# Kernel tuning notes

Measured on AMD Instinct MI355X. Metric: run time of the kernel, lower is better.

Reference implementation:

```python
import jax, jax.numpy as jnp
import numpy as np

B, T, C = 128, 512, 1024  # batch, time (fixed by `line` buffer), channels


def fft_convolve(a, b):
    """Linear convolution via zero-padded FFT, sliced to a's length.
    a: (1, C, T) kernel, b: (B, C, T) signal. Returns (B, C, T)."""
    n = a.shape[-1]
    a_pad = jnp.pad(a, ((0, 0), (0, 0), (0, n)))
    b_pad = jnp.pad(b, ((0, 0), (0, 0), (0, n)))
    spec = jnp.fft.rfft(a_pad, axis=-1) * jnp.fft.rfft(b_pad, axis=-1)
    return jnp.fft.irfft(spec, n=2 * n, axis=-1)[..., :n]


def setup_inputs() -> dict:
    key = jax.random.key(0)
    k1, k2, k3, k4, k5 = jax.random.split(key, 5)
    bound = 1.0 / np.sqrt(C)  # nn.Linear default init range
    x = jax.random.normal(k1, (B, T, C), dtype=jnp.float32)
    W_proj = jax.random.uniform(k2, (C, C), jnp.float32, -bound, bound)
    W_values = jax.random.uniform(k3, (C, C), jnp.float32, -bound, bound)
    gain = jax.random.uniform(k4, (1, 1, C), jnp.float32, 0.01, 1.0)
    pow_ = jax.random.uniform(k5, (1, C, 1), jnp.float32, -6.0, 6.0)
    line = jnp.linspace(1.0, 0.0, T, dtype=jnp.float32)[None, None, :]  # (1,1,T)
    return {"x": x, "W_proj": W_proj, "W_values": W_values,
            "gain": gain, "pow_": pow_, "line": line}


def reference(x, W_proj, W_values, gain, pow_, line):
    # proj and values (bias-free Linears)
    h = jnp.einsum('btc,dc->btd', x, W_proj)          # (B,T,C)
    v = jnp.einsum('btc,dc->btd', h, W_values)        # (B,T,C)
    # learned power-law kernel, one decay per channel: (1,C,T)
    z = line ** (2.0 + jax.nn.sigmoid(pow_) * 100.0)
    # FFT long convolution along time
    y = fft_convolve(z, jnp.transpose(v, (0, 2, 1)))  # (B,C,T)
    y = jnp.transpose(y, (0, 2, 1))                    # (B,T,C)
    return jax.nn.relu(y * gain)
```

## Files before the change

### kernel.cpp

```cpp
#include <hip/hip_runtime.h>
#include <hip/hip_bf16.h>

#define B_ 128
#define T_ 512
#define C_ 1024

typedef __attribute__((ext_vector_type(8))) short short8;
typedef __attribute__((ext_vector_type(4))) float f32x4;

__device__ __forceinline__ unsigned short f2bf(float f){
  unsigned u; __builtin_memcpy(&u, &f, 4);
  u += 0x7FFFu + ((u >> 16) & 1u);
  return (unsigned short)(u >> 16);
}

typedef __attribute__((address_space(3))) unsigned lds_u32_t;
typedef __attribute__((address_space(1))) unsigned glb_u32_t;
typedef __attribute__((address_space(3))) char lds_char;
__device__ __forceinline__ void gload16(const void* g, void* l){
  __builtin_amdgcn_global_load_lds((const glb_u32_t*)g, (lds_u32_t*)l, 16, 0, 0);
}

__global__ void cast_f32_bf16(const float* __restrict__ in, unsigned short* __restrict__ out, long n){
  long i = (long)blockIdx.x * blockDim.x + threadIdx.x;
  long stride = (long)gridDim.x * blockDim.x;
  for (long j = i * 4; j < n; j += stride * 4){
    float4 v = *(const float4*)(in + j);
    ushort4 o; o.x = f2bf(v.x); o.y = f2bf(v.y); o.z = f2bf(v.z); o.w = f2bf(v.w);
    *(ushort4*)(out + j) = o;
  }
}

__global__ void transpose_cast(const float* __restrict__ in, unsigned short* __restrict__ out){
  __shared__ float tile[32][33];
  int c0 = blockIdx.x * 32, e0 = blockIdx.y * 32;
  int tx = threadIdx.x, ty = threadIdx.y;
  for (int r = 0; r < 32; r += 8)
    tile[ty + r][tx] = in[(size_t)(e0 + ty + r) * C_ + c0 + tx];
  __syncthreads();
  for (int r = 0; r < 32; r += 8)
    out[(size_t)(c0 + ty + r) * C_ + e0 + tx] = f2bf(tile[tx][ty + r]);
}

__global__ __launch_bounds__(256) void gemm_bt_bf16(
    const unsigned short* __restrict__ A,
    const unsigned short* __restrict__ Bt,
    unsigned short* __restrict__ Cc,
    int M, int N, int K)
{
  __shared__ short As[128 * 32];
  __shared__ short Bs[128 * 32];
  const int tid  = threadIdx.x;
  const int lane = tid & 63;
  const int wave = tid >> 6;
  const int wr = wave >> 1, wc = wave & 1;
  const int lr = lane & 15, kg = lane >> 4;
  const int m0 = blockIdx.x * 128;
  const int n0 = blockIdx.y * 128;

  f32x4 acc[4][4];
  #pragma unroll
  for (int mi = 0; mi < 4; mi++)
    #pragma unroll
    for (int ni = 0; ni < 4; ni++)
      acc[mi][ni] = (f32x4){0.f, 0.f, 0.f, 0.f};

  const int r1 = tid >> 2, ch1 = tid & 3;
  char* abase = (char*)As + (tid & ~63) * 16;
  char* bbase = (char*)Bs + (tid & ~63) * 16;

  for (int k0 = 0; k0 < K; k0 += 32){
    __syncthreads();
    gload16(A  + (size_t)(m0 + r1)      * K + k0 + ch1 * 8, abase);
    gload16(A  + (size_t)(m0 + 64 + r1) * K + k0 + ch1 * 8, abase + 4096);
    gload16(Bt + (size_t)(n0 + r1)      * K + k0 + ch1 * 8, bbase);
    gload16(Bt + (size_t)(n0 + 64 + r1) * K + k0 + ch1 * 8, bbase + 4096);
    __syncthreads();

    short8 af[4], bfr[4];
    #pragma unroll
    for (int mi = 0; mi < 4; mi++)
      af[mi] = *(const short8*)&As[(wr * 64 + mi * 16 + lr) * 32 + kg * 8];
    #pragma unroll
    for (int ni = 0; ni < 4; ni++)
      bfr[ni] = *(const short8*)&Bs[(wc * 64 + ni * 16 + lr) * 32 + kg * 8];
    #pragma unroll
    for (int mi = 0; mi < 4; mi++)
      #pragma unroll
      for (int ni = 0; ni < 4; ni++)
        acc[mi][ni] = __builtin_amdgcn_mfma_f32_16x16x32_bf16(af[mi], bfr[ni], acc[mi][ni], 0, 0, 0);
  }

  #pragma unroll
  for (int mi = 0; mi < 4; mi++)
    #pragma unroll
    for (int ni = 0; ni < 4; ni++){
      int n = n0 + wc * 64 + ni * 16 + lr;
      int mb = m0 + wr * 64 + mi * 16 + kg * 4;
      #pragma unroll
      for (int j = 0; j < 4; j++)
        Cc[(size_t)(mb + j) * N + n] = f2bf(acc[mi][ni][j]);
    }
}

#define SWZ(x) ((x) ^ ((((x) >> 7) & 3) << 4))

#define STAGE_B(kt, kh) { \
  int d_ = wv * 1024 + ln * 16; int o_ = SWZ(d_); \
  gload16(Bg + (size_t)(n0 + (o_ >> 6)) * 1024 + (kt) * 64 + (kh) * 32 + ((o_ >> 4) & 3) * 8, \
          ldsc + 65536 + ((kt) & 1) * 32768 + (kh) * 16384 + wv * 1024); \
  d_ += 8192; o_ = SWZ(d_); \
  gload16(Bg + (size_t)(n0 + (o_ >> 6)) * 1024 + (kt) * 64 + (kh) * 32 + ((o_ >> 4) & 3) * 8, \
          ldsc + 65536 + ((kt) & 1) * 32768 + (kh) * 16384 + 8192 + wv * 1024); }

#define LOADA(kt) { \
  _Pragma("unroll") for (int kh = 0; kh < 2; kh++) \
    _Pragma("unroll") for (int hf = 0; hf < 2; hf++){ \
      const float* p_ = Ag32 + (size_t)(m0 + rowA + hf * 128) * 1024 + (kt) * 64 + kh * 32 + c8 * 8; \
      areg[kh][hf][0] = *(const float4*)p_; \
      areg[kh][hf][1] = *(const float4*)(p_ + 4); } }

#define CVTWRITE(slot) { \
  _Pragma("unroll") for (int kh = 0; kh < 2; kh++) \
    _Pragma("unroll") for (int hf = 0; hf < 2; hf++){ \
      short8 w_; \
      _Pragma("unroll") for (int q = 0; q < 4; q++){ \
        w_[q]     = (short)f2bf(areg[kh][hf][0][q]); \
        w_[q + 4] = (short)f2bf(areg[kh][hf][1][q]); } \
      int d_ = wv * 1024 + ln * 16 + hf * 8192; \
      unsigned ad_ = (unsigned)(size_t)(lds3 + (slot) * 32768 + kh * 16384 + SWZ(d_)); \
      asm volatile("ds_write_b128 %0, %1" :: "v"(ad_), "v"(w_)); } }

__global__ __launch_bounds__(512, 2) void gemm256_fused(
    const float* __restrict__ Ag32,
    const unsigned short* __restrict__ Bg,
    unsigned short* __restrict__ vt)
{
  extern __shared__ char ldsc[];
  lds_char* lds3 = (lds_char*)ldsc;
  const int tid = threadIdx.x;
  const int ln  = tid & 63;
  const int wv  = tid >> 6;
  const int wr  = wv >> 2;
  const int wc  = wv & 3;
  const int lr  = ln & 15, kg = ln >> 4;
  const int rowA = wv * 16 + (ln >> 2);
  const int c8   = ln & 3;
  const int id  = blockIdx.x;
  const int jj  = (id & 7) * 128 + (id >> 3);
  const int n0  = (jj & 3) * 256;
  const int m0  = (jj >> 2) * 256;

  f32x4 acc[8][4];
  #pragma unroll
  for (int mi = 0; mi < 8; mi++)
    #pragma unroll
    for (int ni = 0; ni < 4; ni++)
      acc[mi][ni] = (f32x4){0.f, 0.f, 0.f, 0.f};

  float4 areg[2][2][2];

  LOADA(0);
  asm volatile("s_waitcnt vmcnt(0)");
  __builtin_amdgcn_sched_barrier(0);
  CVTWRITE(0);
  __builtin_amdgcn_sched_barrier(0);
  STAGE_B(0, 0); STAGE_B(0, 1);
  __builtin_amdgcn_sched_barrier(0);
  asm volatile("s_waitcnt lgkmcnt(0)");
  __builtin_amdgcn_sched_barrier(0);
  asm volatile("s_waitcnt vmcnt(0)");
  __builtin_amdgcn_sched_barrier(0);
  __builtin_amdgcn_s_barrier();

  short8 af[8], bfr[4];

  #pragma unroll 1
  for (int t = 0; t < 16; ++t){
    const int S = t & 1;

    if (t < 15){
      LOADA(t + 1);
      __builtin_amdgcn_sched_barrier(0);
      STAGE_B(t + 1, 0); STAGE_B(t + 1, 1);
      __builtin_amdgcn_sched_barrier(0);
    }

    #pragma unroll
    for (int mi = 0; mi < 8; mi++){
      int off = S * 32768 + (wr * 128 + mi * 16 + lr) * 64 + kg * 16;
      unsigned a_ = (unsigned)(size_t)(lds3 + SWZ(off));
      asm volatile("ds_read_b128 %0, %1" : "=v"(af[mi]) : "v"(a_));
    }
    #pragma unroll
    for (int ni = 0; ni < 4; ni++){
      int off = 65536 + S * 32768 + (wc * 64 + ni * 16 + lr) * 64 + kg * 16;
      unsigned a_ = (unsigned)(size_t)(lds3 + SWZ(off));
      asm volatile("ds_read_b128 %0, %1" : "=v"(bfr[ni]) : "v"(a_));
    }
    asm volatile("s_waitcnt lgkmcnt(0)");
    __builtin_amdgcn_sched_barrier(0);
    __builtin_amdgcn_s_setprio(1);
    #pragma unroll
    for (int mi = 0; mi < 8; mi++)
      #pragma unroll
      for (int ni = 0; ni < 4; ni++)
        acc[mi][ni] = __builtin_amdgcn_mfma_f32_16x16x32_bf16(af[mi], bfr[ni], acc[mi][ni], 0, 0, 0);
    __builtin_amdgcn_s_setprio(0);
    __builtin_amdgcn_sched_barrier(0);

    #pragma unroll
    for (int mi = 0; mi < 8; mi++){
      int off = S * 32768 + 16384 + (wr * 128 + mi * 16 + lr) * 64 + kg * 16;
      unsigned a_ = (unsigned)(size_t)(lds3 + SWZ(off));
      asm volatile("ds_read_b128 %0, %1" : "=v"(af[mi]) : "v"(a_));
    }
    #pragma unroll
    for (int ni = 0; ni < 4; ni++){
      int off = 65536 + S * 32768 + 16384 + (wc * 64 + ni * 16 + lr) * 64 + kg * 16;
      unsigned a_ = (unsigned)(size_t)(lds3 + SWZ(off));
      asm volatile("ds_read_b128 %0, %1" : "=v"(bfr[ni]) : "v"(a_));
    }
    asm volatile("s_waitcnt lgkmcnt(0)");
    __builtin_amdgcn_sched_barrier(0);
    __builtin_amdgcn_s_setprio(1);
    #pragma unroll
    for (int mi = 0; mi < 8; mi++)
      #pragma unroll
      for (int ni = 0; ni < 4; ni++)
        acc[mi][ni] = __builtin_amdgcn_mfma_f32_16x16x32_bf16(af[mi], bfr[ni], acc[mi][ni], 0, 0, 0);
    __builtin_amdgcn_s_setprio(0);
    __builtin_amdgcn_sched_barrier(0);

    if (t < 15){
      asm volatile("s_waitcnt vmcnt(0)");
      __builtin_amdgcn_sched_barrier(0);
      CVTWRITE(S ^ 1);
      __builtin_amdgcn_sched_barrier(0);
      asm volatile("s_waitcnt lgkmcnt(0)");
      __builtin_amdgcn_sched_barrier(0);
    }
    __builtin_amdgcn_s_barrier();
  }

  #pragma unroll
  for (int mi = 0; mi < 8; mi++)
    #pragma unroll
    for (int ni = 0; ni < 4; ni++){
      int n  = n0 + wc * 64 + ni * 16 + lr;
      int mb = m0 + wr * 128 + mi * 16 + kg * 4;
      int bb = mb >> 9, t = mb & 511;
      ushort4 o;
      o.x = f2bf(acc[mi][ni][0]); o.y = f2bf(acc[mi][ni][1]);
      o.z = f2bf(acc[mi][ni][2]); o.w = f2bf(acc[mi][ni][3]);
      *(ushort4*)&vt[((size_t)n * B_ + bb) * T_ + t] = o;
    }
}

__global__ __launch_bounds__(256) void conv_mfma(
    const unsigned short* __restrict__ vt,
    const float* __restrict__ pw,
    const float* __restrict__ line,
    const float* __restrict__ gain,
    unsigned short* __restrict__ Ybf)
{
  __shared__ short Bs[128 * 32];
  __shared__ short Ab[16 * 1280];
  __shared__ unsigned short zbuf[512];
  const int id  = blockIdx.x;
  const int xcd = id & 7;
  const int jj  = id >> 3;
  const int c   = xcd + ((jj >> 2) << 3);
  const int t0  = (jj & 3) << 7;
  const int tid = threadIdx.x, lane = tid & 63, wave = tid >> 6;
  const int wr = wave >> 1, wc = wave & 1, lr = lane & 15, kg = lane >> 4;
  const int K  = t0 + 128;
  const int nb = (t0 >> 5) + 4;

  {
    float p = pw[c];
    float e = 2.0f + 100.0f / (1.0f + expf(-p));
    for (int k = tid; k < K; k += 256){
      float lv = line[k];
      float z = (lv > 0.f) ? expf(e * logf(lv)) : 0.f;
      zbuf[k] = f2bf(z);
    }
  }
  __syncthreads();
  for (int idx = tid; idx < nb * 1280; idx += 256){
    int i = idx / 40, j = idx - i * 40;
    int d32 = i >> 5, ii = i & 31;
    int k = d32 * 32 + ii - j;
    unsigned short v = 0;
    if (j < 32 && k >= 0) v = zbuf[k];
    Ab[idx] = v;
  }

  f32x4 acc[4][4];
  #pragma unroll
  for (int mi = 0; mi < 4; mi++)
    #pragma unroll
    for (int ni = 0; ni < 4; ni++)
      acc[mi][ni] = (f32x4){0.f, 0.f, 0.f, 0.f};

  const int r1 = tid >> 2, ch1 = tid & 3;
  char* bbase = (char*)Bs + (tid & ~63) * 16;
  const size_t vbase = (size_t)c * B_ * T_;

  for (int k0 = 0; k0 < K; k0 += 32){
    __syncthreads();
    gload16(vt + vbase + (size_t)r1 * T_        + k0 + ch1 * 8, bbase);
    gload16(vt + vbase + (size_t)(64 + r1) * T_ + k0 + ch1 * 8, bbase + 4096);
    __syncthreads();

    short8 bfr[4];
    #pragma unroll
    for (int ni = 0; ni < 4; ni++)
      bfr[ni] = *(const short8*)&Bs[(wc * 64 + ni * 16 + lr) * 32 + kg * 8];

    const int dbase = ((t0 - k0) >> 5) + wr * 2;
    #pragma unroll
    for (int mi = 0; mi < 4; mi++){
      const int d32 = dbase + (mi >> 1);
      if (d32 >= 0){
        const int i = ((mi & 1) << 4) + lr;
        short8 af = *(const short8*)&Ab[d32 * 1280 + i * 40 + kg * 8];
        #pragma unroll
        for (int ni = 0; ni < 4; ni++)
          acc[mi][ni] = __builtin_amdgcn_mfma_f32_16x16x32_bf16(af, bfr[ni], acc[mi][ni], 0, 0, 0);
      }
    }
  }

  const float g = gain[c];
  #pragma unroll
  for (int mi = 0; mi < 4; mi++)
    #pragma unroll
    for (int ni = 0; ni < 4; ni++){
      int t = t0 + wr * 64 + mi * 16 + kg * 4;
      int b = wc * 64 + ni * 16 + lr;
      ushort4 o;
      o.x = f2bf(fmaxf(acc[mi][ni][0] * g, 0.f));
      o.y = f2bf(fmaxf(acc[mi][ni][1] * g, 0.f));
      o.z = f2bf(fmaxf(acc[mi][ni][2] * g, 0.f));
      o.w = f2bf(fmaxf(acc[mi][ni][3] * g, 0.f));
      *(ushort4*)&Ybf[((size_t)c * B_ + b) * T_ + t] = o;
    }
}

__global__ __launch_bounds__(256) void final_out(const unsigned short* __restrict__ Ybf,
                                                 float* __restrict__ out){
  __shared__ unsigned short tile[64][72];
  const int c0 = blockIdx.x * 64;
  const int t0 = blockIdx.y * 64;
  const int b  = blockIdx.z;
  const int tid = threadIdx.x;
  const int cr = tid >> 4;
  const int t4 = (tid & 15) * 4;
  for (int q = 0; q < 64; q += 16){
    ushort4 u = *(const ushort4*)&Ybf[((size_t)(c0 + cr + q) * B_ + b) * T_ + t0 + t4];
    *(ushort4*)&tile[cr + q][t4] = u;
  }
  __syncthreads();
  const int tr = tid >> 4;
  const int c4 = (tid & 15) * 4;
  for (int q = 0; q < 64; q += 16){
    int t = tr + q;
    float4 o;
    o.x = __uint_as_float((unsigned)tile[c4 + 0][t] << 16);
    o.y = __uint_as_float((unsigned)tile[c4 + 1][t] << 16);
    o.z = __uint_as_float((unsigned)tile[c4 + 2][t] << 16);
    o.w = __uint_as_float((unsigned)tile[c4 + 3][t] << 16);
    *(float4*)&out[((size_t)b * T_ + t0 + t) * C_ + c0 + c4] = o;
  }
}

extern "C" void kernel_launch(void* const* d_in, const int* in_sizes, int n_in,
                              void* d_out, int out_size, void* d_ws, size_t ws_size,
                              hipStream_t stream)
{
  (void)in_sizes; (void)n_in; (void)out_size; (void)ws_size;
  const float* x    = (const float*)d_in[0];
  const float* Wp   = (const float*)d_in[1];
  const float* Wv   = (const float*)d_in[2];
  const float* gain = (const float*)d_in[3];
  const float* pw   = (const float*)d_in[4];
  const float* line = (const float*)d_in[5];
  float* out = (float*)d_out;

  char* ws = (char*)d_ws;
  unsigned short* Ybf   = (unsigned short*)ws;
  unsigned short* WpT   = (unsigned short*)(ws + 134217728);
  unsigned short* Wv_bf = (unsigned short*)(ws + 134217728 + 2097152);
  unsigned short* W_f   = (unsigned short*)(ws + 134217728 + 2 * 2097152);
  unsigned short* vt    = (unsigned short*)d_out + 67108864;

  cast_f32_bf16<<<256, 256, 0, stream>>>(Wv, Wv_bf, (long)C_ * C_);
  transpose_cast<<<dim3(32, 32), dim3(32, 8), 0, stream>>>(Wp, WpT);
  gemm_bt_bf16<<<dim3(8, 8), 256, 0, stream>>>(Wv_bf, WpT, W_f, C_, C_, C_);
  gemm256_fused<<<1024, 512, 131072, stream>>>(x, W_f, vt);
  conv_mfma<<<4096, 256, 0, stream>>>(vt, pw, line, gain, Ybf);
  final_out<<<dim3(16, 8, 128), 256, 0, stream>>>(Ybf, out);
}
```

Baseline: 447.1 us.

## Pair conv time tiles per block and interleave LDS reads with MFMAs

The causal-convolution kernel now has each block compute two 128-step output tiles, pairing tiles 0 with 2 and 1 with 3. The shared input stream is loaded once and feeds both accumulator sets, which halves the grid, cuts redundant vt loads and Toeplitz setup, and evens out the triangular work per block. The price is double the accumulator registers, which may lower occupancy. In the main GEMM, each half-K step now issues its B then A LDS reads and begins MFMAs per A fragment using staged lgkmcnt waits, so LDS latency overlaps with compute.

Measured after the change: 508.8 us. +13.8%, slower.

```diff
diff --git a/kernel.cpp b/kernel.cpp
--- a/kernel.cpp
+++ b/kernel.cpp
@@ -130,6 +130,32 @@
       int d_ = wv * 1024 + ln * 16 + hf * 8192; \
       unsigned ad_ = (unsigned)(size_t)(lds3 + (slot) * 32768 + kh * 16384 + SWZ(d_)); \
       asm volatile("ds_write_b128 %0, %1" :: "v"(ad_), "v"(w_)); } }
+
+#define MFMA4(MI) { \
+  acc[MI][0] = __builtin_amdgcn_mfma_f32_16x16x32_bf16(af[MI], bfr[0], acc[MI][0], 0, 0, 0); \
+  acc[MI][1] = __builtin_amdgcn_mfma_f32_16x16x32_bf16(af[MI], bfr[1], acc[MI][1], 0, 0, 0); \
+  acc[MI][2] = __builtin_amdgcn_mfma_f32_16x16x32_bf16(af[MI], bfr[2], acc[MI][2], 0, 0, 0); \
+  acc[MI][3] = __builtin_amdgcn_mfma_f32_16x16x32_bf16(af[MI], bfr[3], acc[MI][3], 0, 0, 0); }
+
+#define LSTEP(N, MI) { \
+  asm volatile("s_waitcnt lgkmcnt(" #N ")"); \
+  __builtin_amdgcn_sched_barrier(0); \
+  MFMA4(MI); }
+
+#define KHALF(S, KHOFF) { \
+  _Pragma("unroll") for (int ni = 0; ni < 4; ni++){ \
+    int off = 65536 + (S) * 32768 + (KHOFF) + (wc * 64 + ni * 16 + lr) * 64 + kg * 16; \
+    unsigned a_ = (unsigned)(size_t)(lds3 + SWZ(off)); \
+    asm volatile("ds_read_b128 %0, %1" : "=v"(bfr[ni]) : "v"(a_)); } \
+  _Pragma("unroll") for (int mi = 0; mi < 8; mi++){ \
+    int off = (S) * 32768 + (KHOFF) + (wr * 128 + mi * 16 + lr) * 64 + kg * 16; \
+    unsigned a_ = (unsigned)(size_t)(lds3 + SWZ(off)); \
+    asm volatile("ds_read_b128 %0, %1" : "=v"(af[mi]) : "v"(a_)); } \
+  __builtin_amdgcn_s_setprio(1); \
+  LSTEP(7, 0) LSTEP(6, 1) LSTEP(5, 2) LSTEP(4, 3) \
+  LSTEP(3, 4) LSTEP(2, 5) LSTEP(1, 6) LSTEP(0, 7) \
+  __builtin_amdgcn_s_setprio(0); \
+  __builtin_amdgcn_sched_barrier(0); }
 
 __global__ __launch_bounds__(512, 2) void gemm256_fused(
     const float* __restrict__ Ag32,
@@ -186,51 +212,8 @@
       __builtin_amdgcn_sched_barrier(0);
     }
 
-    #pragma unroll
-    for (int mi = 0; mi < 8; mi++){
-      int off = S * 32768 + (wr * 128 + mi * 16 + lr) * 64 + kg * 16;
-      unsigned a_ = (unsigned)(size_t)(lds3 + SWZ(off));
-      asm volatile("ds_read_b128 %0, %1" : "=v"(af[mi]) : "v"(a_));
-    }
-    #pragma unroll
-    for (int ni = 0; ni < 4; ni++){
-      int off = 65536 + S * 32768 + (wc * 64 + ni * 16 + lr) * 64 + kg * 16;
-      unsigned a_ = (unsigned)(size_t)(lds3 + SWZ(off));
-      asm volatile("ds_read_b128 %0, %1" : "=v"(bfr[ni]) : "v"(a_));
-    }
-    asm volatile("s_waitcnt lgkmcnt(0)");
-    __builtin_amdgcn_sched_barrier(0);
-    __builtin_amdgcn_s_setprio(1);
-    #pragma unroll
-    for (int mi = 0; mi < 8; mi++)
-      #pragma unroll
-      for (int ni = 0; ni < 4; ni++)
-        acc[mi][ni] = __builtin_amdgcn_mfma_f32_16x16x32_bf16(af[mi], bfr[ni], acc[mi][ni], 0, 0, 0);
-    __builtin_amdgcn_s_setprio(0);
-    __builtin_amdgcn_sched_barrier(0);
-
-    #pragma unroll
-    for (int mi = 0; mi < 8; mi++){
-      int off = S * 32768 + 16384 + (wr * 128 + mi * 16 + lr) * 64 + kg * 16;
-      unsigned a_ = (unsigned)(size_t)(lds3 + SWZ(off));
-      asm volatile("ds_read_b128 %0, %1" : "=v"(af[mi]) : "v"(a_));
-    }
-    #pragma unroll
-    for (int ni = 0; ni < 4; ni++){
-      int off = 65536 + S * 32768 + 16384 + (wc * 64 + ni * 16 + lr) * 64 + kg * 16;
-      unsigned a_ = (unsigned)(size_t)(lds3 + SWZ(off));
-      asm volatile("ds_read_b128 %0, %1" : "=v"(bfr[ni]) : "v"(a_));
-    }
-    asm volatile("s_waitcnt lgkmcnt(0)");
-    __builtin_amdgcn_sched_barrier(0);
-    __builtin_amdgcn_s_setprio(1);
-    #pragma unroll
-    for (int mi = 0; mi < 8; mi++)
-      #pragma unroll
-      for (int ni = 0; ni < 4; ni++)
-        acc[mi][ni] = __builtin_amdgcn_mfma_f32_16x16x32_bf16(af[mi], bfr[ni], acc[mi][ni], 0, 0, 0);
-    __builtin_amdgcn_s_setprio(0);
-    __builtin_amdgcn_sched_barrier(0);
+    KHALF(S, 0)
+    KHALF(S, 16384)
 
     if (t < 15){
       asm volatile("s_waitcnt vmcnt(0)");
@@ -257,7 +240,7 @@
     }
 }
 
-__global__ __launch_bounds__(256) void conv_mfma(
+__global__ __launch_bounds__(256) void conv_mfma2(
     const unsigned short* __restrict__ vt,
     const float* __restrict__ pw,
     const float* __restrict__ line,
@@ -270,17 +253,19 @@
   const int id  = blockIdx.x;
   const int xcd = id & 7;
   const int jj  = id >> 3;
-  const int c   = xcd + ((jj >> 2) << 3);
-  const int t0  = (jj & 3) << 7;
+  const int c   = xcd + ((jj >> 1) << 3);
+  const int pr  = jj & 1;
+  const int t0b = pr ? 384 : 128;
+  const int t0a = t0b - 128;
+  const int Kp  = t0b + 128;
   const int tid = threadIdx.x, lane = tid & 63, wave = tid >> 6;
   const int wr = wave >> 1, wc = wave & 1, lr = lane & 15, kg = lane >> 4;
-  const int K  = t0 + 128;
-  const int nb = (t0 >> 5) + 4;
+  const int nb = (t0b >> 5) + 4;
 
   {
     float p = pw[c];
     float e = 2.0f + 100.0f / (1.0f + expf(-p));
-    for (int k = tid; k < K; k += 256){
+    for (int k = tid; k < Kp; k += 256){
       float lv = line[k];
       float z = (lv > 0.f) ? expf(e * logf(lv)) : 0.f;
       zbuf[k] = f2bf(z);
@@ -296,18 +281,20 @@
     Ab[idx] = v;
   }
 
-  f32x4 acc[4][4];
+  f32x4 acca[4][4], accb[4][4];
   #pragma unroll
   for (int mi = 0; mi < 4; mi++)
     #pragma unroll
-    for (int ni = 0; ni < 4; ni++)
-      acc[mi][ni] = (f32x4){0.f, 0.f, 0.f, 0.f};
+    for (int ni = 0; ni < 4; ni++){
+      acca[mi][ni] = (f32x4){0.f, 0.f, 0.f, 0.f};
+      accb[mi][ni] = (f32x4){0.f, 0.f, 0.f, 0.f};
+    }
 
   const int r1 = tid >> 2, ch1 = tid & 3;
   char* bbase = (char*)Bs + (tid & ~63) * 16;
   const size_t vbase = (size_t)c * B_ * T_;
 
-  for (int k0 = 0; k0 < K; k0 += 32){
+  for (int k0 = 0; k0 < Kp; k0 += 32){
     __syncthreads();
     gload16(vt + vbase + (size_t)r1 * T_        + k0 + ch1 * 8, bbase);
     gload16(vt + vbase + (size_t)(64 + r1) * T_ + k0 + ch1 * 8, bbase + 4096);
@@ -318,18 +305,34 @@
     for (int ni = 0; ni < 4; ni++)
       bfr[ni] = *(const short8*)&Bs[(wc * 64 + ni * 16 + lr) * 32 + kg * 8];
 
-    const int dbase = ((t0 - k0) >> 5) + wr * 2;
-    #pragma unroll
-    for (int mi = 0; mi < 4; mi++){
-      const int d32 = dbase + (mi >> 1);
-      if (d32 >= 0){
-        const int i = ((mi & 1) << 4) + lr;
-        short8 af = *(const short8*)&Ab[d32 * 1280 + i * 40 + kg * 8];
-        #pragma unroll
-        for (int ni = 0; ni < 4; ni++)
-          acc[mi][ni] = __builtin_amdgcn_mfma_f32_16x16x32_bf16(af, bfr[ni], acc[mi][ni], 0, 0, 0);
+    {
+      const int dbase = ((t0b - k0) >> 5) + wr * 2;
+      #pragma unroll
+      for (int mi = 0; mi < 4; mi++){
+        const int d32 = dbase + (mi >> 1);
+        if (d32 >= 0){
+          const int i = ((mi & 1) << 4) + lr;
+          short8 afv = *(const short8*)&Ab[d32 * 1280 + i * 40 + kg * 8];
+          #pragma unroll
+          for (int ni = 0; ni < 4; ni++)
+            accb[mi][ni] = __builtin_amdgcn_mfma_f32_16x16x32_bf16(afv, bfr[ni], accb[mi][ni], 0, 0, 0);
+        }
       }
     }
+    if (k0 < t0b){
+      const int dbase = ((t0a - k0) >> 5) + wr * 2;
+      #pragma unroll
+      for (int mi = 0; mi < 4; mi++){
+        const int d32 = dbase + (mi >> 1);
+        if (d32 >= 0){
+          const int i = ((mi & 1) << 4) + lr;
+          short8 afv = *(const short8*)&Ab[d32 * 1280 + i * 40 + kg * 8];
+          #pragma unroll
+          for (int ni = 0; ni < 4; ni++)
+            acca[mi][ni] = __builtin_amdgcn_mfma_f32_16x16x32_bf16(afv, bfr[ni], acca[mi][ni], 0, 0, 0);
+        }
+      }
+    }
   }
 
   const float g = gain[c];
@@ -337,14 +340,20 @@
   for (int mi = 0; mi < 4; mi++)
     #pragma unroll
     for (int ni = 0; ni < 4; ni++){
-      int t = t0 + wr * 64 + mi * 16 + kg * 4;
       int b = wc * 64 + ni * 16 + lr;
-      ushort4 o;
-      o.x = f2bf(fmaxf(acc[mi][ni][0] * g, 0.f));
-      o.y = f2bf(fmaxf(acc[mi][ni][1] * g, 0.f));
-      o.z = f2bf(fmaxf(acc[mi][ni][2] * g, 0.f));
-      o.w = f2bf(fmaxf(acc[mi][ni][3] * g, 0.f));
-      *(ushort4*)&Ybf[((size_t)c * B_ + b) * T_ + t] = o;
+      int ta = t0a + wr * 64 + mi * 16 + kg * 4;
+      int tb = t0b + wr * 64 + mi * 16 + kg * 4;
+      ushort4 oa, ob;
+      oa.x = f2bf(fmaxf(acca[mi][ni][0] * g, 0.f));
+      oa.y = f2bf(fmaxf(acca[mi][ni][1] * g, 0.f));
+      oa.z = f2bf(fmaxf(acca[mi][ni][2] * g, 0.f));
+      oa.w = f2bf(fmaxf(acca[mi][ni][3] * g, 0.f));
+      ob.x = f2bf(fmaxf(accb[mi][ni][0] * g, 0.f));
+      ob.y = f2bf(fmaxf(accb[mi][ni][1] * g, 0.f));
+      ob.z = f2bf(fmaxf(accb[mi][ni][2] * g, 0.f));
+      ob.w = f2bf(fmaxf(accb[mi][ni][3] * g, 0.f));
+      *(ushort4*)&Ybf[((size_t)c * B_ + b) * T_ + ta] = oa;
+      *(ushort4*)&Ybf[((size_t)c * B_ + b) * T_ + tb] = ob;
     }
 }
 
@@ -399,6 +408,6 @@
   transpose_cast<<<dim3(32, 32), dim3(32, 8), 0, stream>>>(Wp, WpT);
   gemm_bt_bf16<<<dim3(8, 8), 256, 0, stream>>>(Wv_bf, WpT, W_f, C_, C_, C_);
   gemm256_fused<<<1024, 512, 131072, stream>>>(x, W_f, vt);
-  conv_mfma<<<4096, 256, 0, stream>>>(vt, pw, line, gain, Ybf);
+  conv_mfma2<<<2048, 256, 0, stream>>>(vt, pw, line, gain, Ybf);
   final_out<<<dim3(16, 8, 128), 256, 0, stream>>>(Ybf, out);
 }
```

## Interleave LDS reads with MFMAs in GEMM and register-prefetch conv tiles

Applied to the files above, without the earlier changes.

In the main GEMM, each K-half now issues its B-fragment reads and then its A-fragment reads, and the MFMA rows start under progressively shrinking lgkmcnt waits, so matrix math begins before every LDS read has landed. The convolution kernel stops using direct global-to-LDS loads with two block barriers per step. It now prefetches the next vt tile into registers during the current step's compute and writes it to LDS at the start of the next step. It also hoists the Toeplitz A-fragment reads ahead of the MFMAs, clamping negative diagonal indices so the reads need no branch. The aim is to hide LDS and global latency behind MFMA work, at the cost of more registers and the added inline-asm ordering constraints.

New measurement: 437.9 us. 1.02x faster.

```diff
diff --git a/kernel.cpp b/kernel.cpp
--- a/kernel.cpp
+++ b/kernel.cpp
@@ -130,6 +130,32 @@
       int d_ = wv * 1024 + ln * 16 + hf * 8192; \
       unsigned ad_ = (unsigned)(size_t)(lds3 + (slot) * 32768 + kh * 16384 + SWZ(d_)); \
       asm volatile("ds_write_b128 %0, %1" :: "v"(ad_), "v"(w_)); } }
+
+#define MFMA4(MI) { \
+  acc[MI][0] = __builtin_amdgcn_mfma_f32_16x16x32_bf16(af[MI], bfr[0], acc[MI][0], 0, 0, 0); \
+  acc[MI][1] = __builtin_amdgcn_mfma_f32_16x16x32_bf16(af[MI], bfr[1], acc[MI][1], 0, 0, 0); \
+  acc[MI][2] = __builtin_amdgcn_mfma_f32_16x16x32_bf16(af[MI], bfr[2], acc[MI][2], 0, 0, 0); \
+  acc[MI][3] = __builtin_amdgcn_mfma_f32_16x16x32_bf16(af[MI], bfr[3], acc[MI][3], 0, 0, 0); }
+
+#define LSTEP(N, MI) { \
+  asm volatile("s_waitcnt lgkmcnt(" #N ")"); \
+  __builtin_amdgcn_sched_barrier(0); \
+  MFMA4(MI); }
+
+#define KHALF(S, KHOFF) { \
+  _Pragma("unroll") for (int ni = 0; ni < 4; ni++){ \
+    int off = 65536 + (S) * 32768 + (KHOFF) + (wc * 64 + ni * 16 + lr) * 64 + kg * 16; \
+    unsigned a_ = (unsigned)(size_t)(lds3 + SWZ(off)); \
+    asm volatile("ds_read_b128 %0, %1" : "=v"(bfr[ni]) : "v"(a_)); } \
+  _Pragma("unroll") for (int mi = 0; mi < 8; mi++){ \
+    int off = (S) * 32768 + (KHOFF) + (wr * 128 + mi * 16 + lr) * 64 + kg * 16; \
+    unsigned a_ = (unsigned)(size_t)(lds3 + SWZ(off)); \
+    asm volatile("ds_read_b128 %0, %1" : "=v"(af[mi]) : "v"(a_)); } \
+  __builtin_amdgcn_s_setprio(1); \
+  LSTEP(7, 0) LSTEP(6, 1) LSTEP(5, 2) LSTEP(4, 3) \
+  LSTEP(3, 4) LSTEP(2, 5) LSTEP(1, 6) LSTEP(0, 7) \
+  __builtin_amdgcn_s_setprio(0); \
+  __builtin_amdgcn_sched_barrier(0); }
 
 __global__ __launch_bounds__(512, 2) void gemm256_fused(
     const float* __restrict__ Ag32,
@@ -186,51 +212,8 @@
       __builtin_amdgcn_sched_barrier(0);
     }
 
-    #pragma unroll
-    for (int mi = 0; mi < 8; mi++){
-      int off = S * 32768 + (wr * 128 + mi * 16 + lr) * 64 + kg * 16;
-      unsigned a_ = (unsigned)(size_t)(lds3 + SWZ(off));
-      asm volatile("ds_read_b128 %0, %1" : "=v"(af[mi]) : "v"(a_));
-    }
-    #pragma unroll
-    for (int ni = 0; ni < 4; ni++){
-      int off = 65536 + S * 32768 + (wc * 64 + ni * 16 + lr) * 64 + kg * 16;
-      unsigned a_ = (unsigned)(size_t)(lds3 + SWZ(off));
-      asm volatile("ds_read_b128 %0, %1" : "=v"(bfr[ni]) : "v"(a_));
-    }
-    asm volatile("s_waitcnt lgkmcnt(0)");
-    __builtin_amdgcn_sched_barrier(0);
-    __builtin_amdgcn_s_setprio(1);
-    #pragma unroll
-    for (int mi = 0; mi < 8; mi++)
-      #pragma unroll
-      for (int ni = 0; ni < 4; ni++)
-        acc[mi][ni] = __builtin_amdgcn_mfma_f32_16x16x32_bf16(af[mi], bfr[ni], acc[mi][ni], 0, 0, 0);
-    __builtin_amdgcn_s_setprio(0);
-    __builtin_amdgcn_sched_barrier(0);
-
-    #pragma unroll
-    for (int mi = 0; mi < 8; mi++){
-      int off = S * 32768 + 16384 + (wr * 128 + mi * 16 + lr) * 64 + kg * 16;
-      unsigned a_ = (unsigned)(size_t)(lds3 + SWZ(off));
-      asm volatile("ds_read_b128 %0, %1" : "=v"(af[mi]) : "v"(a_));
-    }
-    #pragma unroll
-    for (int ni = 0; ni < 4; ni++){
-      int off = 65536 + S * 32768 + 16384 + (wc * 64 + ni * 16 + lr) * 64 + kg * 16;
-      unsigned a_ = (unsigned)(size_t)(lds3 + SWZ(off));
-      asm volatile("ds_read_b128 %0, %1" : "=v"(bfr[ni]) : "v"(a_));
-    }
-    asm volatile("s_waitcnt lgkmcnt(0)");
-    __builtin_amdgcn_sched_barrier(0);
-    __builtin_amdgcn_s_setprio(1);
-    #pragma unroll
-    for (int mi = 0; mi < 8; mi++)
-      #pragma unroll
-      for (int ni = 0; ni < 4; ni++)
-        acc[mi][ni] = __builtin_amdgcn_mfma_f32_16x16x32_bf16(af[mi], bfr[ni], acc[mi][ni], 0, 0, 0);
-    __builtin_amdgcn_s_setprio(0);
-    __builtin_amdgcn_sched_barrier(0);
+    KHALF(S, 0)
+    KHALF(S, 16384)
 
     if (t < 15){
       asm volatile("s_waitcnt vmcnt(0)");
@@ -257,7 +240,7 @@
     }
 }
 
-__global__ __launch_bounds__(256) void conv_mfma(
+__global__ __launch_bounds__(256) void conv_mfma3(
     const unsigned short* __restrict__ vt,
     const float* __restrict__ pw,
     const float* __restrict__ line,
@@ -267,6 +250,8 @@
   __shared__ short Bs[128 * 32];
   __shared__ short Ab[16 * 1280];
   __shared__ unsigned short zbuf[512];
+  lds_char* ldsB = (lds_char*)Bs;
+  lds_char* ldsA = (lds_char*)Ab;
   const int id  = blockIdx.x;
   const int xcd = id & 7;
   const int jj  = id >> 3;
@@ -275,6 +260,7 @@
   const int tid = threadIdx.x, lane = tid & 63, wave = tid >> 6;
   const int wr = wave >> 1, wc = wave & 1, lr = lane & 15, kg = lane >> 4;
   const int K  = t0 + 128;
+  const int nIter = K >> 5;
   const int nb = (t0 >> 5) + 4;
 
   {
@@ -304,32 +290,56 @@
       acc[mi][ni] = (f32x4){0.f, 0.f, 0.f, 0.f};
 
   const int r1 = tid >> 2, ch1 = tid & 3;
-  char* bbase = (char*)Bs + (tid & ~63) * 16;
   const size_t vbase = (size_t)c * B_ * T_;
-
-  for (int k0 = 0; k0 < K; k0 += 32){
-    __syncthreads();
-    gload16(vt + vbase + (size_t)r1 * T_        + k0 + ch1 * 8, bbase);
-    gload16(vt + vbase + (size_t)(64 + r1) * T_ + k0 + ch1 * 8, bbase + 4096);
-    __syncthreads();
-
-    short8 bfr[4];
-    #pragma unroll
-    for (int ni = 0; ni < 4; ni++)
-      bfr[ni] = *(const short8*)&Bs[(wc * 64 + ni * 16 + lr) * 32 + kg * 8];
-
+  const unsigned adw0 = (unsigned)(size_t)(ldsB + tid * 16);
+  const unsigned adw1 = adw0 + 4096;
+
+  short8 va0 = *(const short8*)&vt[vbase + (size_t)r1 * T_        + ch1 * 8];
+  short8 va1 = *(const short8*)&vt[vbase + (size_t)(64 + r1) * T_ + ch1 * 8];
+
+  #pragma unroll 1
+  for (int it = 0; it < nIter; ++it){
+    const int k0 = it << 5;
+    asm volatile("ds_write_b128 %0, %1" :: "v"(adw0), "v"(va0));
+    asm volatile("ds_write_b128 %0, %1" :: "v"(adw1), "v"(va1));
+    asm volatile("s_waitcnt lgkmcnt(0)");
+    __builtin_amdgcn_sched_barrier(0);
+    __builtin_amdgcn_s_barrier();
+
+    if (it + 1 < nIter){
+      va0 = *(const short8*)&vt[vbase + (size_t)r1 * T_        + k0 + 32 + ch1 * 8];
+      va1 = *(const short8*)&vt[vbase + (size_t)(64 + r1) * T_ + k0 + 32 + ch1 * 8];
+    }
+
+    short8 bfr[4], afv[4];
+    #pragma unroll
+    for (int ni = 0; ni < 4; ni++){
+      unsigned a_ = (unsigned)(size_t)(ldsB + (wc * 64 + ni * 16 + lr) * 64 + kg * 16);
+      asm volatile("ds_read_b128 %0, %1" : "=v"(bfr[ni]) : "v"(a_));
+    }
     const int dbase = ((t0 - k0) >> 5) + wr * 2;
     #pragma unroll
     for (int mi = 0; mi < 4; mi++){
-      const int d32 = dbase + (mi >> 1);
-      if (d32 >= 0){
-        const int i = ((mi & 1) << 4) + lr;
-        short8 af = *(const short8*)&Ab[d32 * 1280 + i * 40 + kg * 8];
+      int d32 = dbase + (mi >> 1);
+      int d32c = d32 < 0 ? 0 : d32;
+      int i = ((mi & 1) << 4) + lr;
+      unsigned a_ = (unsigned)(size_t)(ldsA + (d32c * 1280 + i * 40 + kg * 8) * 2);
+      asm volatile("ds_read_b128 %0, %1" : "=v"(afv[mi]) : "v"(a_));
+    }
+    asm volatile("s_waitcnt lgkmcnt(0)");
+    __builtin_amdgcn_sched_barrier(0);
+    __builtin_amdgcn_s_setprio(1);
+    #pragma unroll
+    for (int mi = 0; mi < 4; mi++){
+      if (dbase + (mi >> 1) >= 0){
         #pragma unroll
         for (int ni = 0; ni < 4; ni++)
-          acc[mi][ni] = __builtin_amdgcn_mfma_f32_16x16x32_bf16(af, bfr[ni], acc[mi][ni], 0, 0, 0);
+          acc[mi][ni] = __builtin_amdgcn_mfma_f32_16x16x32_bf16(afv[mi], bfr[ni], acc[mi][ni], 0, 0, 0);
       }
     }
+    __builtin_amdgcn_s_setprio(0);
+    __builtin_amdgcn_sched_barrier(0);
+    __builtin_amdgcn_s_barrier();
   }
 
   const float g = gain[c];
@@ -399,6 +409,6 @@
   transpose_cast<<<dim3(32, 32), dim3(32, 8), 0, stream>>>(Wp, WpT);
   gemm_bt_bf16<<<dim3(8, 8), 256, 0, stream>>>(Wv_bf, WpT, W_f, C_, C_, C_);
   gemm256_fused<<<1024, 512, 131072, stream>>>(x, W_f, vt);
-  conv_mfma<<<4096, 256, 0, stream>>>(vt, pw, line, gain, Ybf);
+  conv_mfma3<<<4096, 256, 0, stream>>>(vt, pw, line, gain, Ybf);
   final_out<<<dim3(16, 8, 128), 256, 0, stream>>>(Ybf, out);
 }
```
